# Optimization experiments

Measured on AMD Instinct MI355X. Metric: run time of the kernel, lower is better.

The kernel has to match this reference:

```python
import jax, jax.numpy as jnp
import numpy as np

B, S, LD, Hh, Ww = 64, 32, 16, 32, 18
D, NH, HD, FF, L = 512, 8, 64, 2048, 6
IN = LD * Hh * Ww  # 9216
EPS = 1e-5


def setup_inputs() -> dict:
    key = jax.random.key(0)
    ks = jax.random.split(key, 8)
    p = lambda k, s: jax.random.normal(k, s, jnp.float32) * 0.02
    return {
        "x": jax.random.normal(ks[0], (B, S, LD, Hh, Ww), jnp.float32),
        "inp_w": p(ks[1], (D, IN)), "inp_b": jnp.zeros((D,), jnp.float32),
        "in_proj_w": p(ks[2], (L, 3 * D, D)), "in_proj_b": jnp.zeros((L, 3 * D), jnp.float32),
        "out_w": p(ks[3], (L, D, D)), "out_b": jnp.zeros((L, D), jnp.float32),
        "ln1_w": jnp.ones((L, D), jnp.float32), "ln1_b": jnp.zeros((L, D), jnp.float32),
        "ln2_w": jnp.ones((L, D), jnp.float32), "ln2_b": jnp.zeros((L, D), jnp.float32),
        "ff1_w": p(ks[4], (L, FF, D)), "ff1_b": jnp.zeros((L, FF), jnp.float32),
        "ff2_w": p(ks[5], (L, D, FF)), "ff2_b": jnp.zeros((L, D), jnp.float32),
        "outp_w": p(ks[6], (IN, D)), "outp_b": jnp.zeros((IN,), jnp.float32),
    }


def _layernorm(x, w, b):
    mu = jnp.mean(x, -1, keepdims=True)
    var = jnp.mean(jnp.square(x - mu), -1, keepdims=True)
    return (x - mu) * jax.lax.rsqrt(var + EPS) * w + b


def _rope(x, cos, sin):
    # x: [B,S,NH,HD]; torchtune interleaved-pair rotation, rope applied BEFORE qk projection
    x2 = x.reshape(*x.shape[:-1], HD // 2, 2)
    x0, x1 = x2[..., 0], x2[..., 1]
    c = cos[None, :, None, :]
    s = sin[None, :, None, :]
    out = jnp.stack([x0 * c - x1 * s, x1 * c + x0 * s], axis=-1)
    return out.reshape(x.shape)


def reference(x, inp_w, inp_b, in_proj_w, in_proj_b, out_w, out_b,
              ln1_w, ln1_b, ln2_w, ln2_b, ff1_w, ff1_b, ff2_w, ff2_b,
              outp_w, outp_b):
    b, s = x.shape[0], x.shape[1]
    h = x.reshape(b, s, IN) @ inp_w.T + inp_b  # [B,S,D]

    theta = 1.0 / (10000.0 ** (jnp.arange(0, HD, 2, dtype=jnp.float32) / HD))
    ang = jnp.arange(s, dtype=jnp.float32)[:, None] * theta  # [S, HD/2]
    cos, sin = jnp.cos(ang), jnp.sin(ang)
    mask = jnp.triu(jnp.full((s, s), -jnp.inf, jnp.float32), k=1)  # causal additive mask
    scale = 1.0 / np.sqrt(HD)

    for i in range(L):
        # RoPE on full hidden state (pre-projection), used for q and k; v uses unrotated h
        hr = _rope(h.reshape(b, s, NH, HD), cos, sin).reshape(b, s, D)
        wq, wk, wv = in_proj_w[i, :D], in_proj_w[i, D:2 * D], in_proj_w[i, 2 * D:]
        bq, bk, bv = in_proj_b[i, :D], in_proj_b[i, D:2 * D], in_proj_b[i, 2 * D:]
        q = (hr @ wq.T + bq).reshape(b, s, NH, HD)
        k = (hr @ wk.T + bk).reshape(b, s, NH, HD)
        v = (h @ wv.T + bv).reshape(b, s, NH, HD)
        scores = jnp.einsum('bqhd,bkhd->bhqk', q, k) * scale + mask
        attn = jax.nn.softmax(scores, axis=-1)
        ctx = jnp.einsum('bhqk,bkhd->bqhd', attn, v).reshape(b, s, D)
        sa = ctx @ out_w[i].T + out_b[i]
        h = _layernorm(h + sa, ln1_w[i], ln1_b[i])  # post-norm (norm_first=False)
        ff = jax.nn.gelu(h @ ff1_w[i].T + ff1_b[i], approximate=False) @ ff2_w[i].T + ff2_b[i]
        h = _layernorm(h + ff, ln2_w[i], ln2_b[i])

    out = h @ outp_w.T + outp_b
    return out.reshape(b, s, LD, Hh, Ww)
```

## Files before the change

kernel.cpp:

```cpp
#include <hip/hip_runtime.h>
#include <hip/hip_bf16.h>
#include <math.h>


typedef __attribute__((ext_vector_type(8))) short bf16x8;
typedef __attribute__((ext_vector_type(4))) short bf16x4;
typedef __attribute__((ext_vector_type(8))) float f32x8;
typedef __attribute__((ext_vector_type(4))) float f32x4;

#define LN_EPS 1e-5f

__device__ inline float bf2f(__hip_bfloat16 v) { return __bfloat162float(v); }
__device__ inline __hip_bfloat16 f2bf(float f) { return __float2bfloat16(f); }

__device__ __forceinline__ void gload_lds16(const __hip_bfloat16* g, __hip_bfloat16* l) {
    __builtin_amdgcn_global_load_lds(
        (const __attribute__((address_space(1))) unsigned*)g,
        (__attribute__((address_space(3))) unsigned*)l, 16, 0, 0);
}

__device__ __forceinline__ void sync_tile() {
    asm volatile("s_waitcnt vmcnt(0) lgkmcnt(0)" ::: "memory");
    __builtin_amdgcn_s_barrier();
    asm volatile("" ::: "memory");
}

__device__ __forceinline__ void sync_lds() {
    asm volatile("s_waitcnt lgkmcnt(0)" ::: "memory");
    __builtin_amdgcn_s_barrier();
    asm volatile("" ::: "memory");
}

struct CvtSeg { const float* src; __hip_bfloat16* dst; };
struct CvtArgs { CvtSeg seg[16]; long cum[17]; };

__global__ __launch_bounds__(256) void convert_all(CvtArgs a, long total8,
                                                   float* __restrict__ rtab) {
    if (blockIdx.x == 0) {
#pragma unroll
        for (int it = 0; it < 4; ++it) {
            const int t = it * 256 + threadIdx.x;
            const int s = t >> 5, p = t & 31;
            const float theta = powf(10000.f, -(float)p / 32.f);
            float sn, cs;
            sincosf((float)s * theta, &sn, &cs);
            rtab[t * 2] = cs;
            rtab[t * 2 + 1] = sn;
        }
    }
    for (long i = (long)blockIdx.x * 256 + threadIdx.x; i < total8;
         i += (long)gridDim.x * 256) {
        int s = 0;
        while (i >= a.cum[s + 1]) ++s;
        const long off = i - a.cum[s];
        const f32x8 x = *((const f32x8*)a.seg[s].src + off);
        union { bf16x8 v; __hip_bfloat16 b[8]; } o;
#pragma unroll
        for (int t = 0; t < 8; ++t) o.b[t] = f2bf(x[t]);
        *((bf16x8*)a.seg[s].dst + off) = o.v;
    }
}

template<int BM, int BN, int EPI, int OUT, int AMODE, int SWZ, int PIPE>
__global__ __launch_bounds__(256) void gemm_bt(
    const void* __restrict__ Araw, int bn_split,
    const float* __restrict__ rtab,
    const __hip_bfloat16* __restrict__ W,
    const __hip_bfloat16* __restrict__ bias,
    void* __restrict__ Cv,
    int M, int N, int Ktot, int KC)
{
    constexpr int FM = BM / 32, FN = BN / 32;
    constexpr int CPT_A = BM / 32, CPT_B = BN / 32;
    constexpr bool REGSTAGE = (AMODE == 3 || AMODE == 4);
    constexpr int NBUF = (PIPE && !REGSTAGE) ? 2 : 1;
    __shared__ __align__(16) __hip_bfloat16 sA[NBUF][BM * 64];
    __shared__ __align__(16) __hip_bfloat16 sB[NBUF][BN * 64];

    const int tid = threadIdx.x, lane = tid & 63, wave = tid >> 6;
    const int wr = wave >> 1, wc = wave & 1;
    const int lr = lane & 15, lk = lane >> 4;

    int bm, bn, zz;
    if (SWZ == 0) {
        const int nbm = gridDim.x, nbn = gridDim.y;
        const int nwg = nbm * nbn;
        const int orig = blockIdx.y * nbm + blockIdx.x;
        const int q8 = nwg >> 3, r8 = nwg & 7;
        const int xcd = orig & 7, loc = orig >> 3;
        const int f = (xcd < r8 ? xcd * (q8 + 1) : r8 * (q8 + 1) + (xcd - r8) * q8) + loc;
        bm = f % nbm; bn = f / nbm; zz = blockIdx.z;
    } else {
        const int bid = blockIdx.x;
        const int xcd = bid & 7, loc = bid >> 3;
        const int nbn = N / BN;
        const int per = (gridDim.x >> 3) / nbn;
        bn = loc % nbn;
        const int gid = xcd * per + loc / nbn;
        bm = gid % (M / BM); zz = gid / (M / BM);
    }
    const int kbeg = zz * KC, kend = kbeg + KC;
    const bool dorot = (AMODE == 2 || AMODE == 4) && (bn < bn_split);

    const __hip_bfloat16* Ab = (const __hip_bfloat16*)Araw + (long)bm * BM * Ktot;
    const float*          Af = (const float*)Araw + (long)bm * BM * Ktot;
    const __hip_bfloat16* Wb = W + (long)bn * BN * Ktot;

    f32x4 acc[FM][FN];
#pragma unroll
    for (int i = 0; i < FM; ++i)
#pragma unroll
        for (int j = 0; j < FN; ++j) acc[i][j] = (f32x4){0.f, 0.f, 0.f, 0.f};

    f32x8  aregf[CPT_A];
    bf16x8 aregb[CPT_A];
    f32x8  csreg[CPT_A];
    bf16x8 bregb[REGSTAGE ? CPT_B : 1];

    auto stageA_g = [&](int buf, int k0) {
#pragma unroll
        for (int c = 0; c < CPT_A; ++c) {
            const int ch = tid + c * 256, row = ch >> 3, co = ch & 7;
            gload_lds16(&Ab[(long)row * Ktot + k0 + ((co ^ (row & 7)) * 8)],
                        (__hip_bfloat16*)((char*)&sA[buf][0] + ch * 16));
        }
    };
    auto stageB_g = [&](int buf, int k0) {
#pragma unroll
        for (int c = 0; c < CPT_B; ++c) {
            const int ch = tid + c * 256, row = ch >> 3, co = ch & 7;
            gload_lds16(&Wb[(long)row * Ktot + k0 + ((co ^ (row & 7)) * 8)],
                        (__hip_bfloat16*)((char*)&sB[buf][0] + ch * 16));
        }
    };
    auto issueA = [&](int k0) {
#pragma unroll
        for (int c = 0; c < CPT_A; ++c) {
            const int ch = tid + c * 256, row = ch >> 3, co = ch & 7;
            if (AMODE == 1 || AMODE == 3)
                aregf[c] = *(const f32x8*)&Af[(long)row * Ktot + k0 + co * 8];
            if (AMODE == 2 || AMODE == 4) {
                aregb[c] = *(const bf16x8*)&Ab[(long)row * Ktot + k0 + co * 8];
                if (dorot)
                    csreg[c] = *(const f32x8*)&rtab[((bm * BM + row) & 31) * 64 + co * 8];
            }
        }
        if (REGSTAGE) {
#pragma unroll
            for (int c = 0; c < CPT_B; ++c) {
                const int ch = tid + c * 256, row = ch >> 3, co = ch & 7;
                bregb[c] = *(const bf16x8*)&Wb[(long)row * Ktot + k0 + co * 8];
            }
        }
    };
    auto writeA = [&](int buf) {
#pragma unroll
        for (int c = 0; c < CPT_A; ++c) {
            const int ch = tid + c * 256, row = ch >> 3, co = ch & 7;
            union { bf16x8 v; __hip_bfloat16 b[8]; } t;
            if (AMODE == 1 || AMODE == 3) {
#pragma unroll
                for (int j = 0; j < 8; ++j) t.b[j] = f2bf(aregf[c][j]);
            } else {
                t.v = aregb[c];
                if (dorot) {
#pragma unroll
                    for (int qd = 0; qd < 4; ++qd) {
                        const float c_ = csreg[c][qd * 2], sn = csreg[c][qd * 2 + 1];
                        const float x0 = bf2f(t.b[2 * qd]);
                        const float x1 = bf2f(t.b[2 * qd + 1]);
                        t.b[2 * qd]     = f2bf(x0 * c_ - x1 * sn);
                        t.b[2 * qd + 1] = f2bf(x1 * c_ + x0 * sn);
                    }
                }
            }
            *(bf16x8*)((char*)&sA[buf][0] + row * 128 + ((co ^ (row & 7)) << 4)) = t.v;
        }
        if (REGSTAGE) {
#pragma unroll
            for (int c = 0; c < CPT_B; ++c) {
                const int ch = tid + c * 256, row = ch >> 3, co = ch & 7;
                *(bf16x8*)((char*)&sB[buf][0] + row * 128 + ((co ^ (row & 7)) << 4)) = bregb[c];
            }
        }
    };
    auto compute = [&](int buf) {
        bf16x8 af[2][FM], bfr[2][FN];
#pragma unroll
        for (int ks = 0; ks < 2; ++ks) {
#pragma unroll
            for (int i = 0; i < FM; ++i) {
                const int row = wr * (BM / 2) + i * 16 + lr;
                const int co = ks * 4 + lk;
                af[ks][i] = *(const bf16x8*)((const char*)&sA[buf][0] + row * 128 +
                                             ((co ^ (row & 7)) << 4));
            }
#pragma unroll
            for (int j = 0; j < FN; ++j) {
                const int row = wc * (BN / 2) + j * 16 + lr;
                const int co = ks * 4 + lk;
                bfr[ks][j] = *(const bf16x8*)((const char*)&sB[buf][0] + row * 128 +
                                              ((co ^ (row & 7)) << 4));
            }
        }
#pragma unroll
        for (int ks = 0; ks < 2; ++ks)
#pragma unroll
            for (int i = 0; i < FM; ++i)
#pragma unroll
                for (int j = 0; j < FN; ++j)
                    acc[i][j] = __builtin_amdgcn_mfma_f32_16x16x32_bf16(
                        af[ks][i], bfr[ks][j], acc[i][j], 0, 0, 0);
    };

    if (REGSTAGE) {
        issueA(kbeg);
        for (int k0 = kbeg; k0 < kend; k0 += 64) {
            if (k0 > kbeg) __builtin_amdgcn_s_barrier();
            writeA(0);
            sync_lds();
            if (k0 + 64 < kend) issueA(k0 + 64);
            compute(0);
        }
    } else if (PIPE == 0) {
        if (AMODE != 0) issueA(kbeg);
        for (int k0 = kbeg; k0 < kend; k0 += 64) {
            if (k0 > kbeg) __builtin_amdgcn_s_barrier();
            if (AMODE == 0) stageA_g(0, k0);
            stageB_g(0, k0);
            if (AMODE != 0) writeA(0);
            sync_tile();
            if (AMODE != 0 && k0 + 64 < kend) issueA(k0 + 64);
            compute(0);
        }
    } else {
        if (AMODE == 0) stageA_g(0, kbeg); else issueA(kbeg);
        stageB_g(0, kbeg);
        if (AMODE != 0) writeA(0);
        sync_tile();
        int cur = 0;
        for (int k0 = kbeg; k0 < kend; k0 += 64) {
            const bool hn = (k0 + 64 < kend);
            if (hn) {
                if (AMODE == 0) stageA_g(cur ^ 1, k0 + 64); else issueA(k0 + 64);
                stageB_g(cur ^ 1, k0 + 64);
            }
            compute(cur);
            if (hn) {
                if (AMODE != 0) writeA(cur ^ 1);
                sync_tile();
            }
            cur ^= 1;
        }
    }

    const int row0 = bm * BM + wr * (BM / 2);
    const int col0 = bn * BN + wc * (BN / 2);
    if (OUT == 1) {
        float* Cp = (float*)Cv + (long)zz * M * N;
#pragma unroll
        for (int i = 0; i < FM; ++i)
#pragma unroll
            for (int j = 0; j < FN; ++j) {
                const int col = col0 + j * 16 + lr;
#pragma unroll
                for (int r = 0; r < 4; ++r)
                    Cp[(long)(row0 + i * 16 + lk * 4 + r) * N + col] = acc[i][j][r];
            }
    } else {
#pragma unroll
        for (int i = 0; i < FM; ++i)
#pragma unroll
            for (int j = 0; j < FN; ++j) {
                const int col = col0 + j * 16 + lr;
                const float bv = bf2f(bias[col]);
#pragma unroll
                for (int r = 0; r < 4; ++r) {
                    const int row = row0 + i * 16 + lk * 4 + r;
                    float v = acc[i][j][r] + bv;
                    if (EPI == 1) v = 0.5f * v * (1.0f + erff(v * 0.70710678118654752f));
                    const long idx = (long)row * N + col;
                    if (OUT == 2) ((float*)Cv)[idx] = v;
                    else          ((__hip_bfloat16*)Cv)[idx] = f2bf(v);
                }
            }
    }
}

template<int SK>
__global__ __launch_bounds__(256) void sk_reduce(
    const float* __restrict__ part, const __hip_bfloat16* __restrict__ bias,
    __hip_bfloat16* __restrict__ out)
{
    const long MN = 2048L * 512;
    const long i4 = ((long)blockIdx.x * 256 + threadIdx.x) * 4;
    f32x4 s = (f32x4){0.f, 0.f, 0.f, 0.f};
#pragma unroll
    for (int z = 0; z < SK; ++z) s += *(const f32x4*)&part[z * MN + i4];
    const int col = (int)(i4 & 511);
    union { bf16x4 v; __hip_bfloat16 b[4]; } o;
#pragma unroll
    for (int j = 0; j < 4; ++j) o.b[j] = f2bf(s[j] + bf2f(bias[col + j]));
    *(bf16x4*)&out[i4] = o.v;
}

template<int SK>
__global__ __launch_bounds__(256) void skred_add_ln(
    const float* __restrict__ part, const __hip_bfloat16* __restrict__ bias,
    const __hip_bfloat16* __restrict__ resid,
    const __hip_bfloat16* __restrict__ w, const __hip_bfloat16* __restrict__ b,
    __hip_bfloat16* __restrict__ out)
{
    const long MN = 2048L * 512;
    const int wave = threadIdx.x >> 6, lane = threadIdx.x & 63;
    const long row = (long)blockIdx.x * 4 + wave;
    const long base = row * 512 + lane * 8;

    f32x8 acc = *(const f32x8*)&part[base];
#pragma unroll
    for (int z = 1; z < SK; ++z) acc += *(const f32x8*)&part[z * MN + base];

    union { bf16x8 v; __hip_bfloat16 b[8]; } ur, uo;
    ur.v = *(const bf16x8*)&resid[base];

    float x[8];
    float s = 0.f, s2 = 0.f;
#pragma unroll
    for (int j = 0; j < 8; ++j) {
        const int col = lane * 8 + j;
        x[j] = acc[j] + bf2f(bias[col]) + bf2f(ur.b[j]);
        s += x[j];
        s2 += x[j] * x[j];
    }
#pragma unroll
    for (int off = 32; off; off >>= 1) {
        s  += __shfl_xor(s, off);
        s2 += __shfl_xor(s2, off);
    }
    const float mu = s * (1.f / 512.f);
    const float var = s2 * (1.f / 512.f) - mu * mu;
    const float rs = rsqrtf(var + LN_EPS);
#pragma unroll
    for (int j = 0; j < 8; ++j) {
        const int col = lane * 8 + j;
        uo.b[j] = f2bf((x[j] - mu) * rs * bf2f(w[col]) + bf2f(b[col]));
    }
    *(bf16x8*)&out[base] = uo.v;
}

__global__ __launch_bounds__(256) void attn_mfma(
    const __hip_bfloat16* __restrict__ qkv, __hip_bfloat16* __restrict__ ctx)
{
    __shared__ __align__(16) __hip_bfloat16 sP[4][32 * 32];
    __shared__ __align__(16) __hip_bfloat16 sVT[4][64 * 32];

    const int wave = threadIdx.x >> 6, lane = threadIdx.x & 63;
    const int bh = blockIdx.x * 4 + wave;
    const int b = bh >> 3, head = bh & 7;
    const long tok0 = (long)b * 32;
    const int lr = lane & 15, lk = lane >> 4;

    const __hip_bfloat16* Qb = qkv + tok0 * 1536 + head * 64;
    const __hip_bfloat16* Kb = Qb + 512;
    const __hip_bfloat16* Vb = Qb + 1024;

#pragma unroll
    for (int t = 0; t < 4; ++t) {
        const int c = lane + t * 64, row = c >> 3, d0 = (c & 7) * 8;
        union { bf16x8 v; __hip_bfloat16 e[8]; } u;
        u.v = *(const bf16x8*)&Vb[(long)row * 1536 + d0];
#pragma unroll
        for (int e = 0; e < 8; ++e) sVT[wave][(d0 + e) * 32 + row] = u.e[e];
    }

    f32x4 sc[2][2];
#pragma unroll
    for (int i = 0; i < 2; ++i)
#pragma unroll
        for (int j = 0; j < 2; ++j) sc[i][j] = (f32x4){0.f, 0.f, 0.f, 0.f};
#pragma unroll
    for (int ks = 0; ks < 2; ++ks) {
        bf16x8 aq[2], bk[2];
#pragma unroll
        for (int i = 0; i < 2; ++i)
            aq[i] = *(const bf16x8*)&Qb[(long)(i * 16 + lr) * 1536 + ks * 32 + lk * 8];
#pragma unroll
        for (int j = 0; j < 2; ++j)
            bk[j] = *(const bf16x8*)&Kb[(long)(j * 16 + lr) * 1536 + ks * 32 + lk * 8];
#pragma unroll
        for (int i = 0; i < 2; ++i)
#pragma unroll
            for (int j = 0; j < 2; ++j)
                sc[i][j] = __builtin_amdgcn_mfma_f32_16x16x32_bf16(aq[i], bk[j], sc[i][j], 0, 0, 0);
    }

    float p[2][2][4], inv[2][4];
#pragma unroll
    for (int i = 0; i < 2; ++i) {
#pragma unroll
        for (int r = 0; r < 4; ++r) {
            const int row = i * 16 + lk * 4 + r;
            float m = -3.0e38f;
#pragma unroll
            for (int j = 0; j < 2; ++j) {
                const int col = j * 16 + lr;
                const float v = (col <= row) ? sc[i][j][r] * 0.125f : -3.0e38f;
                p[i][j][r] = v;
                m = fmaxf(m, v);
            }
#pragma unroll
            for (int off = 1; off < 16; off <<= 1)
                m = fmaxf(m, __shfl_xor(m, off));
            float l = 0.f;
#pragma unroll
            for (int j = 0; j < 2; ++j) {
                p[i][j][r] = expf(p[i][j][r] - m);
                l += p[i][j][r];
            }
#pragma unroll
            for (int off = 1; off < 16; off <<= 1)
                l += __shfl_xor(l, off);
            inv[i][r] = 1.f / l;
        }
    }

#pragma unroll
    for (int i = 0; i < 2; ++i)
#pragma unroll
        for (int j = 0; j < 2; ++j)
#pragma unroll
            for (int r = 0; r < 4; ++r)
                sP[wave][(i * 16 + lk * 4 + r) * 32 + j * 16 + lr] = f2bf(p[i][j][r]);

    bf16x8 pa[2], vb[4];
#pragma unroll
    for (int i = 0; i < 2; ++i)
        pa[i] = *(const bf16x8*)&sP[wave][(i * 16 + lr) * 32 + lk * 8];
#pragma unroll
    for (int j = 0; j < 4; ++j)
        vb[j] = *(const bf16x8*)&sVT[wave][(j * 16 + lr) * 32 + lk * 8];

    f32x4 o[2][4];
#pragma unroll
    for (int i = 0; i < 2; ++i)
#pragma unroll
        for (int j = 0; j < 4; ++j) {
            o[i][j] = (f32x4){0.f, 0.f, 0.f, 0.f};
            o[i][j] = __builtin_amdgcn_mfma_f32_16x16x32_bf16(pa[i], vb[j], o[i][j], 0, 0, 0);
        }

#pragma unroll
    for (int i = 0; i < 2; ++i)
#pragma unroll
        for (int j = 0; j < 4; ++j) {
            const int col = j * 16 + lr;
#pragma unroll
            for (int r = 0; r < 4; ++r) {
                const int row = i * 16 + lk * 4 + r;
                ctx[(tok0 + row) * 512 + head * 64 + col] = f2bf(o[i][j][r] * inv[i][r]);
            }
        }
}

extern "C" void kernel_launch(void* const* d_in, const int* in_sizes, int n_in,
                              void* d_out, int out_size, void* d_ws, size_t ws_size,
                              hipStream_t stream)
{
    const int M = 2048;
    __hip_bfloat16* wts = (__hip_bfloat16*)d_ws;

    const long O_INPW   = 0;
    const long O_INPROJ = 4718592;
    const long O_OUTW   = 9437184;
    const long O_FF1    = 11010048;
    const long O_FF2    = 17301504;
    const long O_OUTPW  = 23592960;
    const long O_INPB   = 28311552;
    const long O_INPROJB= 28312064;
    const long O_OUTB   = 28321280;
    const long O_LN1W   = 28324352;
    const long O_LN1B   = 28327424;
    const long O_LN2W   = 28330496;
    const long O_LN2B   = 28333568;
    const long O_FF1B   = 28336640;
    const long O_FF2B   = 28348928;
    const long O_OUTPB  = 28352000;
    const long O_ACT    = 28361216;

    __hip_bfloat16* h   = wts + O_ACT;
    __hip_bfloat16* ht  = h   + (long)M * 512;
    __hip_bfloat16* qkv = ht  + (long)M * 512;
    __hip_bfloat16* ctx = qkv + (long)M * 1536;
    __hip_bfloat16* ffh = ctx + (long)M * 512;
    float* rtab = (float*)(ffh + (long)M * 2048);
    float* skpart = (float*)((__hip_bfloat16*)rtab + 4096);

    const int  cidx[16] = {1, 3, 5, 11, 13, 15, 2, 4, 6, 7, 8, 9, 10, 12, 14, 16};
    const long coff[16] = {O_INPW, O_INPROJ, O_OUTW, O_FF1, O_FF2, O_OUTPW,
                           O_INPB, O_INPROJB, O_OUTB, O_LN1W, O_LN1B, O_LN2W,
                           O_LN2B, O_FF1B, O_FF2B, O_OUTPB};
    const long csz[16]  = {4718592, 4718592, 1572864, 6291456, 6291456, 4718592,
                           512, 9216, 3072, 3072, 3072, 3072, 3072, 12288, 3072, 9216};
    CvtArgs ca;
    long cum = 0;
    for (int s = 0; s < 16; ++s) {
        ca.seg[s].src = (const float*)d_in[cidx[s]];
        ca.seg[s].dst = wts + coff[s];
        ca.cum[s] = cum;
        cum += csz[s] / 8;
    }
    ca.cum[16] = cum;
    convert_all<<<2048, 256, 0, stream>>>(ca, cum, rtab);

    gemm_bt<64, 256, 0, 1, 3, 1, 0><<<512, 256, 0, stream>>>(
        d_in[0], 0, rtab, wts + O_INPW, wts + O_INPB, skpart, M, 512, 9216, 1152);
    sk_reduce<8><<<1024, 256, 0, stream>>>(skpart, wts + O_INPB, h);

    for (int i = 0; i < 6; ++i) {
        const __hip_bfloat16* wqkv = wts + O_INPROJ + (long)i * 1536 * 512;
        const __hip_bfloat16* bqkv = wts + O_INPROJB + i * 1536;

        gemm_bt<64, 64, 0, 0, 4, 0, 0><<<dim3(32, 24), 256, 0, stream>>>(
            h, 16, rtab, wqkv, bqkv, qkv, M, 1536, 512, 512);
        attn_mfma<<<128, 256, 0, stream>>>(qkv, ctx);
        gemm_bt<64, 64, 0, 1, 4, 0, 0><<<dim3(32, 8, 2), 256, 0, stream>>>(
            ctx, 0, rtab, wts + O_OUTW + (long)i * 512 * 512, wts + O_OUTB + i * 512,
            skpart, M, 512, 512, 256);
        skred_add_ln<2><<<512, 256, 0, stream>>>(
            skpart, wts + O_OUTB + i * 512, h,
            wts + O_LN1W + i * 512, wts + O_LN1B + i * 512, ht);
        gemm_bt<64, 64, 1, 0, 4, 0, 0><<<dim3(32, 32), 256, 0, stream>>>(
            ht, 0, rtab, wts + O_FF1 + (long)i * 2048 * 512, wts + O_FF1B + i * 2048,
            ffh, M, 2048, 512, 512);
        gemm_bt<64, 64, 0, 1, 4, 0, 0><<<dim3(32, 8, 4), 256, 0, stream>>>(
            ffh, 0, rtab, wts + O_FF2 + (long)i * 512 * 2048, wts + O_FF2B + i * 512,
            skpart, M, 512, 2048, 512);
        skred_add_ln<4><<<512, 256, 0, stream>>>(
            skpart, wts + O_FF2B + i * 512, ht,
            wts + O_LN2W + i * 512, wts + O_LN2B + i * 512, h);
    }

    gemm_bt<128, 128, 0, 2, 4, 0, 0><<<dim3(16, 72), 256, 0, stream>>>(
        h, 0, rtab, wts + O_OUTPW, wts + O_OUTPB, d_out, M, 9216, 512, 512);
}
```

Before: 473.9 us.

## Double-buffer register prefetch in input projection GEMM and unroll conversion loop

Adds AMODE 5, which keeps two register sets of A (fp32) and B tiles so global loads are issued two k-steps ahead. The large split-K input projection GEMM uses it, which should hide more memory latency on its 9216-wide K loop. The fp32-to-bf16 conversion kernel also handles two elements per iteration, giving more loads in flight. The cost is higher register pressure in the GEMM, which could reduce occupancy.

Measured after the change: 591.1 us. 1.25x slower.

```diff
diff --git a/kernel.cpp b/kernel.cpp
--- a/kernel.cpp
+++ b/kernel.cpp
@@ -48,16 +48,31 @@
             rtab[t * 2 + 1] = sn;
         }
     }
-    for (long i = (long)blockIdx.x * 256 + threadIdx.x; i < total8;
-         i += (long)gridDim.x * 256) {
-        int s = 0;
-        while (i >= a.cum[s + 1]) ++s;
-        const long off = i - a.cum[s];
-        const f32x8 x = *((const f32x8*)a.seg[s].src + off);
-        union { bf16x8 v; __hip_bfloat16 b[8]; } o;
-#pragma unroll
-        for (int t = 0; t < 8; ++t) o.b[t] = f2bf(x[t]);
-        *((bf16x8*)a.seg[s].dst + off) = o.v;
+    const long st = (long)gridDim.x * 256;
+    for (long i = (long)blockIdx.x * 256 + threadIdx.x; i < total8; i += 2 * st) {
+        int s1 = 0;
+        while (i >= a.cum[s1 + 1]) ++s1;
+        const long o1 = i - a.cum[s1];
+        const f32x8 x1 = *((const f32x8*)a.seg[s1].src + o1);
+
+        const long j = i + st;
+        if (j < total8) {
+            int s2 = s1;
+            while (j >= a.cum[s2 + 1]) ++s2;
+            const long o2 = j - a.cum[s2];
+            const f32x8 x2 = *((const f32x8*)a.seg[s2].src + o2);
+
+            union { bf16x8 v; __hip_bfloat16 b[8]; } u1, u2;
+#pragma unroll
+            for (int t = 0; t < 8; ++t) { u1.b[t] = f2bf(x1[t]); u2.b[t] = f2bf(x2[t]); }
+            *((bf16x8*)a.seg[s1].dst + o1) = u1.v;
+            *((bf16x8*)a.seg[s2].dst + o2) = u2.v;
+        } else {
+            union { bf16x8 v; __hip_bfloat16 b[8]; } u1;
+#pragma unroll
+            for (int t = 0; t < 8; ++t) u1.b[t] = f2bf(x1[t]);
+            *((bf16x8*)a.seg[s1].dst + o1) = u1.v;
+        }
     }
 }
 
@@ -72,7 +87,8 @@
 {
     constexpr int FM = BM / 32, FN = BN / 32;
     constexpr int CPT_A = BM / 32, CPT_B = BN / 32;
-    constexpr bool REGSTAGE = (AMODE == 3 || AMODE == 4);
+    constexpr bool REGSTAGE = (AMODE == 3 || AMODE == 4 || AMODE == 5);
+    constexpr int NSET = (AMODE == 5) ? 2 : 1;
     constexpr int NBUF = (PIPE && !REGSTAGE) ? 2 : 1;
     __shared__ __align__(16) __hip_bfloat16 sA[NBUF][BM * 64];
     __shared__ __align__(16) __hip_bfloat16 sB[NBUF][BN * 64];
@@ -112,10 +128,10 @@
 #pragma unroll
         for (int j = 0; j < FN; ++j) acc[i][j] = (f32x4){0.f, 0.f, 0.f, 0.f};
 
-    f32x8  aregf[CPT_A];
+    f32x8  aregf[NSET][CPT_A];
     bf16x8 aregb[CPT_A];
     f32x8  csreg[CPT_A];
-    bf16x8 bregb[REGSTAGE ? CPT_B : 1];
+    bf16x8 bregb[REGSTAGE ? NSET : 1][REGSTAGE ? CPT_B : 1];
 
     auto stageA_g = [&](int buf, int k0) {
 #pragma unroll
@@ -133,12 +149,12 @@
                         (__hip_bfloat16*)((char*)&sB[buf][0] + ch * 16));
         }
     };
-    auto issueA = [&](int k0) {
+    auto issueA = [&](int k0, int set) {
 #pragma unroll
         for (int c = 0; c < CPT_A; ++c) {
             const int ch = tid + c * 256, row = ch >> 3, co = ch & 7;
-            if (AMODE == 1 || AMODE == 3)
-                aregf[c] = *(const f32x8*)&Af[(long)row * Ktot + k0 + co * 8];
+            if (AMODE == 1 || AMODE == 3 || AMODE == 5)
+                aregf[set][c] = *(const f32x8*)&Af[(long)row * Ktot + k0 + co * 8];
             if (AMODE == 2 || AMODE == 4) {
                 aregb[c] = *(const bf16x8*)&Ab[(long)row * Ktot + k0 + co * 8];
                 if (dorot)
@@ -149,18 +165,18 @@
 #pragma unroll
             for (int c = 0; c < CPT_B; ++c) {
                 const int ch = tid + c * 256, row = ch >> 3, co = ch & 7;
-                bregb[c] = *(const bf16x8*)&Wb[(long)row * Ktot + k0 + co * 8];
+                bregb[set][c] = *(const bf16x8*)&Wb[(long)row * Ktot + k0 + co * 8];
             }
         }
     };
-    auto writeA = [&](int buf) {
+    auto writeA = [&](int buf, int set) {
 #pragma unroll
         for (int c = 0; c < CPT_A; ++c) {
             const int ch = tid + c * 256, row = ch >> 3, co = ch & 7;
             union { bf16x8 v; __hip_bfloat16 b[8]; } t;
-            if (AMODE == 1 || AMODE == 3) {
-#pragma unroll
-                for (int j = 0; j < 8; ++j) t.b[j] = f2bf(aregf[c][j]);
+            if (AMODE == 1 || AMODE == 3 || AMODE == 5) {
+#pragma unroll
+                for (int j = 0; j < 8; ++j) t.b[j] = f2bf(aregf[set][c][j]);
             } else {
                 t.v = aregb[c];
                 if (dorot) {
@@ -180,7 +196,8 @@
 #pragma unroll
             for (int c = 0; c < CPT_B; ++c) {
                 const int ch = tid + c * 256, row = ch >> 3, co = ch & 7;
-                *(bf16x8*)((char*)&sB[buf][0] + row * 128 + ((co ^ (row & 7)) << 4)) = bregb[c];
+                *(bf16x8*)((char*)&sB[buf][0] + row * 128 + ((co ^ (row & 7)) << 4)) =
+                    bregb[set][c];
             }
         }
     };
@@ -213,41 +230,53 @@
                         af[ks][i], bfr[ks][j], acc[i][j], 0, 0, 0);
     };
 
-    if (REGSTAGE) {
-        issueA(kbeg);
+    if (AMODE == 5) {
+        issueA(kbeg, 0);
+        if (kbeg + 64 < kend) issueA(kbeg + 64, 1);
+        int t = 0;
+        for (int k0 = kbeg; k0 < kend; k0 += 64, ++t) {
+            if (t > 0) __builtin_amdgcn_s_barrier();
+            const int set = t & 1;
+            writeA(0, set);
+            sync_lds();
+            if (k0 + 128 < kend) issueA(k0 + 128, set);
+            compute(0);
+        }
+    } else if (REGSTAGE) {
+        issueA(kbeg, 0);
         for (int k0 = kbeg; k0 < kend; k0 += 64) {
             if (k0 > kbeg) __builtin_amdgcn_s_barrier();
-            writeA(0);
+            writeA(0, 0);
             sync_lds();
-            if (k0 + 64 < kend) issueA(k0 + 64);
+            if (k0 + 64 < kend) issueA(k0 + 64, 0);
             compute(0);
         }
     } else if (PIPE == 0) {
-        if (AMODE != 0) issueA(kbeg);
+        if (AMODE != 0) issueA(kbeg, 0);
         for (int k0 = kbeg; k0 < kend; k0 += 64) {
             if (k0 > kbeg) __builtin_amdgcn_s_barrier();
             if (AMODE == 0) stageA_g(0, k0);
             stageB_g(0, k0);
-            if (AMODE != 0) writeA(0);
+            if (AMODE != 0) writeA(0, 0);
             sync_tile();
-            if (AMODE != 0 && k0 + 64 < kend) issueA(k0 + 64);
+            if (AMODE != 0 && k0 + 64 < kend) issueA(k0 + 64, 0);
             compute(0);
         }
     } else {
-        if (AMODE == 0) stageA_g(0, kbeg); else issueA(kbeg);
+        if (AMODE == 0) stageA_g(0, kbeg); else issueA(kbeg, 0);
         stageB_g(0, kbeg);
-        if (AMODE != 0) writeA(0);
+        if (AMODE != 0) writeA(0, 0);
         sync_tile();
         int cur = 0;
         for (int k0 = kbeg; k0 < kend; k0 += 64) {
             const bool hn = (k0 + 64 < kend);
             if (hn) {
-                if (AMODE == 0) stageA_g(cur ^ 1, k0 + 64); else issueA(k0 + 64);
+                if (AMODE == 0) stageA_g(cur ^ 1, k0 + 64); else issueA(k0 + 64, 0);
                 stageB_g(cur ^ 1, k0 + 64);
             }
             compute(cur);
             if (hn) {
-                if (AMODE != 0) writeA(cur ^ 1);
+                if (AMODE != 0) writeA(cur ^ 1, 0);
                 sync_tile();
             }
             cur ^= 1;
@@ -512,7 +541,7 @@
     ca.cum[16] = cum;
     convert_all<<<2048, 256, 0, stream>>>(ca, cum, rtab);
 
-    gemm_bt<64, 256, 0, 1, 3, 1, 0><<<512, 256, 0, stream>>>(
+    gemm_bt<64, 256, 0, 1, 5, 1, 0><<<512, 256, 0, stream>>>(
         d_in[0], 0, rtab, wts + O_INPW, wts + O_INPB, skpart, M, 512, 9216, 1152);
     sk_reduce<8><<<1024, 256, 0, stream>>>(skpart, wts + O_INPB, h);
 
```
